# Kernel tuning notes

Hardware: AMD Instinct MI355X
Metric: run time of the kernel (lower is better)

The kernel has to match this reference:

```python
import jax, jax.numpy as jnp
import numpy as np

N_HEADS = 16
WINDOW = 256  # window_size; keep keys with |i-j| <= WINDOW//2


def setup_inputs() -> dict:
    key = jax.random.key(0)
    ks = jax.random.split(key, 6)
    B, S, D = 2, 2048, 1024
    x = jax.random.normal(ks[0], (B, S, D), dtype=jnp.float32)
    # torch nn.Linear weights are [out_features, in_features]
    scale = 1.0 / np.sqrt(D)
    Wq = jax.random.normal(ks[1], (D, D), dtype=jnp.float32) * scale
    Wk = jax.random.normal(ks[2], (D, D), dtype=jnp.float32) * scale
    Wv = jax.random.normal(ks[3], (D, D), dtype=jnp.float32) * scale
    Wo = jax.random.normal(ks[4], (D, D), dtype=jnp.float32) * scale
    # standard ALiBi slopes: 2^(-8*(h+1)/H)
    slopes = jnp.asarray(2.0 ** (-8.0 * (np.arange(1, N_HEADS + 1) / N_HEADS)), dtype=jnp.float32)
    return {"x": x, "Wq": Wq, "Wk": Wk, "Wv": Wv, "Wo": Wo, "slopes": slopes}


def reference(x, Wq, Wk, Wv, Wo, slopes):
    B, S, D = x.shape
    H = N_HEADS
    dk = D // H
    # projections (torch Linear: y = x @ W.T)
    q = jnp.einsum('bsd,od->bso', x, Wq).reshape(B, S, H, dk)
    k = jnp.einsum('bsd,od->bso', x, Wk).reshape(B, S, H, dk)
    v = jnp.einsum('bsd,od->bso', x, Wv).reshape(B, S, H, dk)
    # full score matrix [B,H,S,S]
    scores = jnp.einsum('bqhd,bkhd->bhqk', q, k) / jnp.sqrt(jnp.asarray(dk, x.dtype))
    pos = jnp.arange(S)
    rel = (pos[:, None] - pos[None, :]).astype(x.dtype)          # [S,S] q_pos - k_pos
    scores = scores + slopes[None, :, None, None] * rel[None, None]
    window_mask = jnp.abs(pos[:, None] - pos[None, :]) <= (WINDOW // 2)  # [S,S]
    scores = jnp.where(window_mask[None, None], scores, -jnp.inf)
    attn = jax.nn.softmax(scores, axis=-1)
    out = jnp.einsum('bhqk,bkhd->bqhd', attn, v).reshape(B, S, D)
    return jnp.einsum('bsd,od->bso', out, Wo)
```

## Files before the change

kernel.cpp:

```cpp
#include <hip/hip_runtime.h>
#include <hip/hip_bf16.h>

#define S_LEN   2048
#define D_MODEL 1024
#define NH      16
#define DK      64
#define BATCH   2
#define M_ROWS  (BATCH * S_LEN)
#define LDP     72

typedef __attribute__((ext_vector_type(8))) short bf16x8;
typedef __attribute__((ext_vector_type(4))) float f32x4;
typedef __attribute__((ext_vector_type(8))) unsigned short us8;

static __device__ __forceinline__ float b2f(unsigned short s) {
    unsigned u = ((unsigned)s) << 16;
    return __builtin_bit_cast(float, u);
}
static __device__ __forceinline__ unsigned short f2bf(float f) {
    unsigned u = __builtin_bit_cast(unsigned, f);
    u += 0x7fffu + ((u >> 16) & 1u);
    return (unsigned short)(u >> 16);
}

__global__ __launch_bounds__(256) void cvt_bf16(const float* __restrict__ src,
                                                unsigned short* __restrict__ dst, int n8) {
    int i = blockIdx.x * 256 + threadIdx.x;
    if (i >= n8) return;
    const float4* s = (const float4*)src + (size_t)i * 2;
    float4 a = s[0], b = s[1];
    us8 o;
    o[0] = f2bf(a.x); o[1] = f2bf(a.y); o[2] = f2bf(a.z); o[3] = f2bf(a.w);
    o[4] = f2bf(b.x); o[5] = f2bf(b.y); o[6] = f2bf(b.z); o[7] = f2bf(b.w);
    *((us8*)dst + i) = o;
}

__global__ __launch_bounds__(256) void cvt_bf16_w4(const float* __restrict__ s0,
                                                   const float* __restrict__ s1,
                                                   const float* __restrict__ s2,
                                                   const float* __restrict__ s3,
                                                   unsigned short* __restrict__ dst) {
    const int which = blockIdx.x >> 9;
    const float* src = (which == 0) ? s0 : (which == 1) ? s1 : (which == 2) ? s2 : s3;
    const int i = (blockIdx.x & 511) * 256 + threadIdx.x;
    const float4* s = (const float4*)src + (size_t)i * 2;
    float4 a = s[0], b = s[1];
    us8 o;
    o[0] = f2bf(a.x); o[1] = f2bf(a.y); o[2] = f2bf(a.z); o[3] = f2bf(a.w);
    o[4] = f2bf(b.x); o[5] = f2bf(b.y); o[6] = f2bf(b.z); o[7] = f2bf(b.w);
    *((us8*)(dst + (size_t)which * 1024 * 1024) + i) = o;
}

template <int STORE_BF16>
__global__ __launch_bounds__(256) void mfma_gemm_bt(const unsigned short* __restrict__ A,
                                                    const unsigned short* __restrict__ W,
                                                    void* __restrict__ Cv, int N) {
    constexpr int K = 1024, BM = 128, BN = 128, BK = 64;
    __shared__ unsigned short As[BM * BK];
    __shared__ unsigned short Bs[BN * BK];

    const int tid  = threadIdx.x;
    const int w    = tid >> 6;
    const int lane = tid & 63;
    const int m0 = blockIdx.y * BM;
    const int n0 = blockIdx.x * BN;
    const int wr = (w >> 1) * 64;
    const int wc = (w & 1) * 64;

    const int srow   = lane >> 3;
    const int schunk = ((lane & 7) ^ (lane >> 3)) * 8;

    const int sw = lane & 7;
    const int c0 = (((lane >> 4) + 0) ^ sw) * 8;
    const int c1 = (((lane >> 4) + 4) ^ sw) * 8;

    f32x4 acc[4][4] = {};

    for (int k0 = 0; k0 < K; k0 += BK) {
        __syncthreads();
#pragma unroll
        for (int t = 0; t < 4; ++t) {
            const int rbase = w * 32 + t * 8;
            const unsigned short* ga = A + (size_t)(m0 + rbase + srow) * K + k0 + schunk;
            __builtin_amdgcn_global_load_lds(
                (const __attribute__((address_space(1))) void*)ga,
                (__attribute__((address_space(3))) void*)(As + rbase * BK), 16, 0, 0);
            const unsigned short* gb = W + (size_t)(n0 + rbase + srow) * K + k0 + schunk;
            __builtin_amdgcn_global_load_lds(
                (const __attribute__((address_space(1))) void*)gb,
                (__attribute__((address_space(3))) void*)(Bs + rbase * BK), 16, 0, 0);
        }
        __syncthreads();

        const int fr = lane & 15;
#pragma unroll
        for (int kk = 0; kk < 2; ++kk) {
            const int co = kk ? c1 : c0;
            bf16x8 af[4], bfr[4];
#pragma unroll
            for (int i = 0; i < 4; ++i)
                af[i] = *(const bf16x8*)(As + (wr + i * 16 + fr) * BK + co);
#pragma unroll
            for (int j = 0; j < 4; ++j)
                bfr[j] = *(const bf16x8*)(Bs + (wc + j * 16 + fr) * BK + co);
#pragma unroll
            for (int i = 0; i < 4; ++i)
#pragma unroll
                for (int j = 0; j < 4; ++j)
                    acc[i][j] = __builtin_amdgcn_mfma_f32_16x16x32_bf16(af[i], bfr[j], acc[i][j], 0, 0, 0);
        }
    }

    const int col = lane & 15;
    const int rq  = (lane >> 4) * 4;
#pragma unroll
    for (int i = 0; i < 4; ++i)
#pragma unroll
        for (int j = 0; j < 4; ++j)
#pragma unroll
            for (int r = 0; r < 4; ++r) {
                const int gm = m0 + wr + i * 16 + rq + r;
                const int gn = n0 + wc + j * 16 + col;
                if (STORE_BF16)
                    ((unsigned short*)Cv)[(size_t)gm * N + gn] = f2bf(acc[i][j][r]);
                else
                    ((float*)Cv)[(size_t)gm * N + gn] = acc[i][j][r];
            }
}

__global__ __launch_bounds__(256) void attn_mfma(const unsigned short* __restrict__ qkvb,
                                                 const float* __restrict__ slopes,
                                                 unsigned short* __restrict__ aoutb) {
    __shared__ unsigned short Qs[64 * LDP];
    __shared__ unsigned short Ks[64 * LDP];
    __shared__ unsigned short Vt[64 * LDP];
    __shared__ unsigned short Ps[64 * LDP];

    const int tid  = threadIdx.x;
    const int w    = tid >> 6;
    const int lane = tid & 63;
    const int q0 = blockIdx.x * 64;
    const int h  = blockIdx.y;
    const int b  = blockIdx.z;
    const float slope = slopes[h];
    const size_t rowbase = (size_t)b * S_LEN * 3072;

#pragma unroll
    for (int e = 0; e < 2; ++e) {
        int idx = e * 256 + tid;
        int r = idx >> 3, cc = (idx & 7) * 8;
        us8 v = *(const us8*)(qkvb + rowbase + (size_t)(q0 + r) * 3072 + h * DK + cc);
        *(us8*)(Qs + r * LDP + cc) = v;
    }

    const int col = lane & 15;
    const int rq  = (lane >> 4) * 4;
    const int wq  = w * 16;
    const int fo  = (lane >> 4) * 8;

    f32x4 o_acc[4] = {};
    float m_i[4], l_i[4];
#pragma unroll
    for (int r = 0; r < 4; ++r) { m_i[r] = -1e30f; l_i[r] = 0.f; }

    for (int c = 0; c < 5; ++c) {
        const int k0 = q0 - 128 + c * 64;
        __syncthreads();

#pragma unroll
        for (int e = 0; e < 2; ++e) {
            int idx = e * 256 + tid;
            int r = idx >> 3, cc = (idx & 7) * 8;
            int kpos = k0 + r;
            us8 kv = {0, 0, 0, 0, 0, 0, 0, 0};
            if ((unsigned)kpos < (unsigned)S_LEN)
                kv = *(const us8*)(qkvb + rowbase + (size_t)kpos * 3072 + 1024 + h * DK + cc);
            *(us8*)(Ks + r * LDP + cc) = kv;
        }
        {
            int rp = tid >> 3;
            int cc = (tid & 7) * 8;
            int kp0 = k0 + rp * 2;
            us8 v0 = {0, 0, 0, 0, 0, 0, 0, 0}, v1 = {0, 0, 0, 0, 0, 0, 0, 0};
            if ((unsigned)kp0 < (unsigned)S_LEN)
                v0 = *(const us8*)(qkvb + rowbase + (size_t)kp0 * 3072 + 2048 + h * DK + cc);
            if ((unsigned)(kp0 + 1) < (unsigned)S_LEN)
                v1 = *(const us8*)(qkvb + rowbase + (size_t)(kp0 + 1) * 3072 + 2048 + h * DK + cc);
#pragma unroll
            for (int t = 0; t < 8; ++t) {
                unsigned pk = (unsigned)(unsigned short)v0[t] | ((unsigned)(unsigned short)v1[t] << 16);
                *(unsigned*)(Vt + (cc + t) * LDP + rp * 2) = pk;
            }
        }
        __syncthreads();

        f32x4 sacc[4] = {};
        {
            bf16x8 aq0 = *(const bf16x8*)(Qs + (wq + col) * LDP + fo);
            bf16x8 aq1 = *(const bf16x8*)(Qs + (wq + col) * LDP + fo + 32);
#pragma unroll
            for (int j = 0; j < 4; ++j) {
                bf16x8 bk0 = *(const bf16x8*)(Ks + (j * 16 + col) * LDP + fo);
                bf16x8 bk1 = *(const bf16x8*)(Ks + (j * 16 + col) * LDP + fo + 32);
                sacc[j] = __builtin_amdgcn_mfma_f32_16x16x32_bf16(aq0, bk0, sacc[j], 0, 0, 0);
                sacc[j] = __builtin_amdgcn_mfma_f32_16x16x32_bf16(aq1, bk1, sacc[j], 0, 0, 0);
            }
        }

        float sv[4][4];
#pragma unroll
        for (int j = 0; j < 4; ++j) {
            const int kpos = k0 + j * 16 + col;
            const bool kin = (unsigned)kpos < (unsigned)S_LEN;
#pragma unroll
            for (int r = 0; r < 4; ++r) {
                const int rel = (q0 + wq + rq + r) - kpos;
                const bool ok = kin && (rel <= 128) && (rel >= -128);
                sv[j][r] = ok ? (sacc[j][r] * 0.125f + slope * (float)rel) : -1e30f;
            }
        }

#pragma unroll
        for (int r = 0; r < 4; ++r) {
            float mx = fmaxf(fmaxf(sv[0][r], sv[1][r]), fmaxf(sv[2][r], sv[3][r]));
#pragma unroll
            for (int off = 1; off < 16; off <<= 1) mx = fmaxf(mx, __shfl_xor(mx, off, 64));
            const float mnew = fmaxf(m_i[r], mx);
            const float alpha = __expf(m_i[r] - mnew);
            float ps = 0.f;
#pragma unroll
            for (int j = 0; j < 4; ++j) {
                float p = (sv[j][r] < -9e29f) ? 0.f : __expf(sv[j][r] - mnew);
                sv[j][r] = p;
                ps += p;
            }
#pragma unroll
            for (int off = 1; off < 16; off <<= 1) ps += __shfl_xor(ps, off, 64);
            l_i[r] = l_i[r] * alpha + ps;
            m_i[r] = mnew;
#pragma unroll
            for (int j = 0; j < 4; ++j) o_acc[j][r] *= alpha;
        }

#pragma unroll
        for (int j = 0; j < 4; ++j)
#pragma unroll
            for (int r = 0; r < 4; ++r)
                Ps[(wq + rq + r) * LDP + j * 16 + col] = f2bf(sv[j][r]);
        __syncthreads();

        {
            bf16x8 ap0 = *(const bf16x8*)(Ps + (wq + col) * LDP + fo);
            bf16x8 ap1 = *(const bf16x8*)(Ps + (wq + col) * LDP + fo + 32);
#pragma unroll
            for (int j = 0; j < 4; ++j) {
                bf16x8 bv0 = *(const bf16x8*)(Vt + (j * 16 + col) * LDP + fo);
                bf16x8 bv1 = *(const bf16x8*)(Vt + (j * 16 + col) * LDP + fo + 32);
                o_acc[j] = __builtin_amdgcn_mfma_f32_16x16x32_bf16(ap0, bv0, o_acc[j], 0, 0, 0);
                o_acc[j] = __builtin_amdgcn_mfma_f32_16x16x32_bf16(ap1, bv1, o_acc[j], 0, 0, 0);
            }
        }
    }

    float inv[4];
#pragma unroll
    for (int r = 0; r < 4; ++r) inv[r] = 1.f / l_i[r];
#pragma unroll
    for (int j = 0; j < 4; ++j)
#pragma unroll
        for (int r = 0; r < 4; ++r) {
            const int qpos = q0 + wq + rq + r;
            aoutb[((size_t)b * S_LEN + qpos) * D_MODEL + h * DK + j * 16 + col] =
                f2bf(o_acc[j][r] * inv[r]);
        }
}

extern "C" void kernel_launch(void* const* d_in, const int* in_sizes, int n_in,
                              void* d_out, int out_size, void* d_ws, size_t ws_size,
                              hipStream_t stream) {
    const float* x      = (const float*)d_in[0];
    const float* Wq     = (const float*)d_in[1];
    const float* Wk     = (const float*)d_in[2];
    const float* Wv     = (const float*)d_in[3];
    const float* Wo     = (const float*)d_in[4];
    const float* slopes = (const float*)d_in[5];
    float* out = (float*)d_out;

    unsigned short* xb    = (unsigned short*)d_ws;
    unsigned short* wb    = xb    + (size_t)M_ROWS * D_MODEL;
    unsigned short* wob   = wb    + (size_t)3072 * D_MODEL;
    unsigned short* qkvb  = wob   + (size_t)1024 * D_MODEL;
    unsigned short* aoutb = qkvb  + (size_t)M_ROWS * 3072;

    dim3 blk(256);
    cvt_bf16<<<2048, blk, 0, stream>>>(x, xb, M_ROWS * D_MODEL / 8);
    cvt_bf16_w4<<<2048, blk, 0, stream>>>(Wq, Wk, Wv, Wo, wb);
    mfma_gemm_bt<1><<<dim3(3072 / 128, M_ROWS / 128), blk, 0, stream>>>(xb, wb, qkvb, 3072);
    attn_mfma<<<dim3(S_LEN / 64, NH, BATCH), blk, 0, stream>>>(qkvb, slopes, aoutb);
    mfma_gemm_bt<0><<<dim3(1024 / 128, M_ROWS / 128), blk, 0, stream>>>(aoutb, wob, out, 1024);
}
```

Measured before the change: 173.7 us.

## Fuse converts, coalesce QKV GEMM stores via LDS, narrow out-proj tile, drop attn barrier

Merges the x and weight bf16 conversion kernels into a single launch. The QKV GEMM epilogue now stages bf16 results in padded shared memory and writes 16-byte coalesced rows instead of scattered 2-byte stores. The output projection uses a 128x64 tile to double the block count for better CU occupancy. A __syncthreads between writing and reading the P tile in attention is removed, relying on each wave only touching its own rows.

```diff
diff --git a/kernel.cpp b/kernel.cpp
--- a/kernel.cpp
+++ b/kernel.cpp
@@ -8,10 +8,12 @@
 #define BATCH   2
 #define M_ROWS  (BATCH * S_LEN)
 #define LDP     72
+#define LDW     132
 
 typedef __attribute__((ext_vector_type(8))) short bf16x8;
 typedef __attribute__((ext_vector_type(4))) float f32x4;
 typedef __attribute__((ext_vector_type(8))) unsigned short us8;
+typedef __attribute__((ext_vector_type(4))) unsigned short us4;
 
 static __device__ __forceinline__ float b2f(unsigned short s) {
     unsigned u = ((unsigned)s) << 16;
@@ -23,58 +25,61 @@
     return (unsigned short)(u >> 16);
 }
 
-__global__ __launch_bounds__(256) void cvt_bf16(const float* __restrict__ src,
-                                                unsigned short* __restrict__ dst, int n8) {
-    int i = blockIdx.x * 256 + threadIdx.x;
-    if (i >= n8) return;
-    const float4* s = (const float4*)src + (size_t)i * 2;
-    float4 a = s[0], b = s[1];
-    us8 o;
-    o[0] = f2bf(a.x); o[1] = f2bf(a.y); o[2] = f2bf(a.z); o[3] = f2bf(a.w);
-    o[4] = f2bf(b.x); o[5] = f2bf(b.y); o[6] = f2bf(b.z); o[7] = f2bf(b.w);
-    *((us8*)dst + i) = o;
-}
-
-__global__ __launch_bounds__(256) void cvt_bf16_w4(const float* __restrict__ s0,
-                                                   const float* __restrict__ s1,
-                                                   const float* __restrict__ s2,
-                                                   const float* __restrict__ s3,
-                                                   unsigned short* __restrict__ dst) {
-    const int which = blockIdx.x >> 9;
-    const float* src = (which == 0) ? s0 : (which == 1) ? s1 : (which == 2) ? s2 : s3;
-    const int i = (blockIdx.x & 511) * 256 + threadIdx.x;
-    const float4* s = (const float4*)src + (size_t)i * 2;
-    float4 a = s[0], b = s[1];
-    us8 o;
-    o[0] = f2bf(a.x); o[1] = f2bf(a.y); o[2] = f2bf(a.z); o[3] = f2bf(a.w);
-    o[4] = f2bf(b.x); o[5] = f2bf(b.y); o[6] = f2bf(b.z); o[7] = f2bf(b.w);
-    *((us8*)(dst + (size_t)which * 1024 * 1024) + i) = o;
-}
-
-template <int STORE_BF16>
+__global__ __launch_bounds__(256) void cvt_all(const float* __restrict__ x,
+                                               const float* __restrict__ wq,
+                                               const float* __restrict__ wk,
+                                               const float* __restrict__ wv,
+                                               const float* __restrict__ wo,
+                                               unsigned short* __restrict__ dst) {
+    const int b = blockIdx.x;
+    if (b < 2048) {
+        const size_t o8 = (size_t)b * 256 + threadIdx.x;
+        const float4* s = (const float4*)x + o8 * 2;
+        float4 a = s[0], bb = s[1];
+        us8 o;
+        o[0] = f2bf(a.x);  o[1] = f2bf(a.y);  o[2] = f2bf(a.z);  o[3] = f2bf(a.w);
+        o[4] = f2bf(bb.x); o[5] = f2bf(bb.y); o[6] = f2bf(bb.z); o[7] = f2bf(bb.w);
+        *((us8*)dst + o8) = o;
+    } else {
+        const int wi = (b - 2048) >> 9;
+        const float* src = (wi == 0) ? wq : (wi == 1) ? wk : (wi == 2) ? wv : wo;
+        const size_t local = (size_t)((b - 2048) & 511) * 256 + threadIdx.x;
+        const float4* s = (const float4*)src + local * 2;
+        float4 a = s[0], bb = s[1];
+        us8 o;
+        o[0] = f2bf(a.x);  o[1] = f2bf(a.y);  o[2] = f2bf(a.z);  o[3] = f2bf(a.w);
+        o[4] = f2bf(bb.x); o[5] = f2bf(bb.y); o[6] = f2bf(bb.z); o[7] = f2bf(bb.w);
+        *((us8*)dst + 524288 + (size_t)wi * 131072 + local) = o;
+    }
+}
+
+template <int STORE_BF16, int BN>
 __global__ __launch_bounds__(256) void mfma_gemm_bt(const unsigned short* __restrict__ A,
                                                     const unsigned short* __restrict__ W,
                                                     void* __restrict__ Cv, int N) {
-    constexpr int K = 1024, BM = 128, BN = 128, BK = 64;
-    __shared__ unsigned short As[BM * BK];
-    __shared__ unsigned short Bs[BN * BK];
+    constexpr int K = 1024, BM = 128, BK = 64;
+    constexpr int MI = (BN == 128) ? 4 : 2;
+    constexpr int SMEM = (STORE_BF16 && BN == 128) ? (128 * LDW)
+                                                   : (BM * BK + BN * BK);
+    __shared__ unsigned short smem[SMEM];
+    unsigned short* As = smem;
+    unsigned short* Bs = smem + BM * BK;
 
     const int tid  = threadIdx.x;
     const int w    = tid >> 6;
     const int lane = tid & 63;
     const int m0 = blockIdx.y * BM;
     const int n0 = blockIdx.x * BN;
-    const int wr = (w >> 1) * 64;
-    const int wc = (w & 1) * 64;
+    const int wr = (BN == 128) ? (w >> 1) * 64 : w * 32;
+    const int wc = (BN == 128) ? (w & 1) * 64 : 0;
 
     const int srow   = lane >> 3;
     const int schunk = ((lane & 7) ^ (lane >> 3)) * 8;
-
     const int sw = lane & 7;
     const int c0 = (((lane >> 4) + 0) ^ sw) * 8;
     const int c1 = (((lane >> 4) + 4) ^ sw) * 8;
 
-    f32x4 acc[4][4] = {};
+    f32x4 acc[MI][4] = {};
 
     for (int k0 = 0; k0 < K; k0 += BK) {
         __syncthreads();
@@ -85,6 +90,10 @@
             __builtin_amdgcn_global_load_lds(
                 (const __attribute__((address_space(1))) void*)ga,
                 (__attribute__((address_space(3))) void*)(As + rbase * BK), 16, 0, 0);
+        }
+#pragma unroll
+        for (int t = 0; t < BN / 32; ++t) {
+            const int rbase = w * (BN / 4) + t * 8;
             const unsigned short* gb = W + (size_t)(n0 + rbase + srow) * K + k0 + schunk;
             __builtin_amdgcn_global_load_lds(
                 (const __attribute__((address_space(1))) void*)gb,
@@ -96,15 +105,15 @@
 #pragma unroll
         for (int kk = 0; kk < 2; ++kk) {
             const int co = kk ? c1 : c0;
-            bf16x8 af[4], bfr[4];
-#pragma unroll
-            for (int i = 0; i < 4; ++i)
+            bf16x8 af[MI], bfr[4];
+#pragma unroll
+            for (int i = 0; i < MI; ++i)
                 af[i] = *(const bf16x8*)(As + (wr + i * 16 + fr) * BK + co);
 #pragma unroll
             for (int j = 0; j < 4; ++j)
                 bfr[j] = *(const bf16x8*)(Bs + (wc + j * 16 + fr) * BK + co);
 #pragma unroll
-            for (int i = 0; i < 4; ++i)
+            for (int i = 0; i < MI; ++i)
 #pragma unroll
                 for (int j = 0; j < 4; ++j)
                     acc[i][j] = __builtin_amdgcn_mfma_f32_16x16x32_bf16(af[i], bfr[j], acc[i][j], 0, 0, 0);
@@ -113,19 +122,44 @@
 
     const int col = lane & 15;
     const int rq  = (lane >> 4) * 4;
-#pragma unroll
-    for (int i = 0; i < 4; ++i)
-#pragma unroll
-        for (int j = 0; j < 4; ++j)
-#pragma unroll
-            for (int r = 0; r < 4; ++r) {
-                const int gm = m0 + wr + i * 16 + rq + r;
-                const int gn = n0 + wc + j * 16 + col;
-                if (STORE_BF16)
-                    ((unsigned short*)Cv)[(size_t)gm * N + gn] = f2bf(acc[i][j][r]);
-                else
-                    ((float*)Cv)[(size_t)gm * N + gn] = acc[i][j][r];
-            }
+
+    if constexpr (STORE_BF16 && BN == 128) {
+        __syncthreads();
+#pragma unroll
+        for (int i = 0; i < 4; ++i)
+#pragma unroll
+            for (int j = 0; j < 4; ++j)
+#pragma unroll
+                for (int r = 0; r < 4; ++r)
+                    smem[(wr + i * 16 + rq + r) * LDW + wc + j * 16 + col] = f2bf(acc[i][j][r]);
+        __syncthreads();
+#pragma unroll
+        for (int e = 0; e < 8; ++e) {
+            const int idx = e * 256 + tid;
+            const int row = idx >> 4;
+            const int cc  = (idx & 15) * 8;
+            us4 lo = *(const us4*)(smem + row * LDW + cc);
+            us4 hi = *(const us4*)(smem + row * LDW + cc + 4);
+            us8 v;
+            v[0] = lo[0]; v[1] = lo[1]; v[2] = lo[2]; v[3] = lo[3];
+            v[4] = hi[0]; v[5] = hi[1]; v[6] = hi[2]; v[7] = hi[3];
+            *(us8*)((unsigned short*)Cv + (size_t)(m0 + row) * N + n0 + cc) = v;
+        }
+    } else {
+#pragma unroll
+        for (int i = 0; i < MI; ++i)
+#pragma unroll
+            for (int j = 0; j < 4; ++j)
+#pragma unroll
+                for (int r = 0; r < 4; ++r) {
+                    const int gm = m0 + wr + i * 16 + rq + r;
+                    const int gn = n0 + wc + j * 16 + col;
+                    if (STORE_BF16)
+                        ((unsigned short*)Cv)[(size_t)gm * N + gn] = f2bf(acc[i][j][r]);
+                    else
+                        ((float*)Cv)[(size_t)gm * N + gn] = acc[i][j][r];
+                }
+    }
 }
 
 __global__ __launch_bounds__(256) void attn_mfma(const unsigned short* __restrict__ qkvb,
@@ -247,7 +281,6 @@
 #pragma unroll
             for (int r = 0; r < 4; ++r)
                 Ps[(wq + rq + r) * LDP + j * 16 + col] = f2bf(sv[j][r]);
-        __syncthreads();
 
         {
             bf16x8 ap0 = *(const bf16x8*)(Ps + (wq + col) * LDP + fo);
@@ -293,9 +326,8 @@
     unsigned short* aoutb = qkvb  + (size_t)M_ROWS * 3072;
 
     dim3 blk(256);
-    cvt_bf16<<<2048, blk, 0, stream>>>(x, xb, M_ROWS * D_MODEL / 8);
-    cvt_bf16_w4<<<2048, blk, 0, stream>>>(Wq, Wk, Wv, Wo, wb);
-    mfma_gemm_bt<1><<<dim3(3072 / 128, M_ROWS / 128), blk, 0, stream>>>(xb, wb, qkvb, 3072);
+    cvt_all<<<4096, blk, 0, stream>>>(x, Wq, Wk, Wv, Wo, xb);
+    mfma_gemm_bt<1, 128><<<dim3(3072 / 128, M_ROWS / 128), blk, 0, stream>>>(xb, wb, qkvb, 3072);
     attn_mfma<<<dim3(S_LEN / 64, NH, BATCH), blk, 0, stream>>>(qkvb, slopes, aoutb);
-    mfma_gemm_bt<0><<<dim3(1024 / 128, M_ROWS / 128), blk, 0, stream>>>(aoutb, wob, out, 1024);
-}
+    mfma_gemm_bt<0, 64><<<dim3(1024 / 64, M_ROWS / 128), blk, 0, stream>>>(aoutb, wob, out, 1024);
+}
```

After: 159.6 us. -8.1%, faster.
